# Optimization experiments

Measured on AMD Instinct MI355X. Metric: run time of the kernel, lower is better.

The kernel has to match this reference:

```python
import jax, jax.numpy as jnp
import numpy as np

N_NODES = 100000
N_EDGES = 1600000
D_IN = 128
D_HID = 128
D_OUT = 1
N_GRAPHS = 512


def setup_inputs() -> dict:
    key = jax.random.key(0)
    ks = jax.random.split(key, 12)
    x = jax.random.normal(ks[0], (N_NODES, D_IN), dtype=jnp.float32)
    edge_index = jax.random.randint(ks[1], (2, N_EDGES), 0, N_NODES, dtype=jnp.int32)
    batch = jnp.sort(jax.random.randint(ks[2], (N_NODES,), 0, N_GRAPHS, dtype=jnp.int32))

    def glorot(k, fan_in, fan_out):
        lim = jnp.sqrt(6.0 / (fan_in + fan_out)).astype(jnp.float32)
        return jax.random.uniform(k, (fan_in, fan_out), jnp.float32, -lim, lim)

    W1 = glorot(ks[3], D_IN, D_HID); b1 = jnp.zeros((D_HID,), jnp.float32)
    W2 = glorot(ks[4], D_HID, D_HID); b2 = jnp.zeros((D_HID,), jnp.float32)
    W3 = glorot(ks[5], D_HID, D_HID); b3 = jnp.zeros((D_HID,), jnp.float32)
    Wfc = glorot(ks[6], D_HID, D_OUT); bfc = jnp.zeros((D_OUT,), jnp.float32)
    return {"x": x, "edge_index": edge_index, "batch": batch,
            "W1": W1, "b1": b1, "W2": W2, "b2": b2, "W3": W3, "b3": b3,
            "Wfc": Wfc, "bfc": bfc}


def reference(x, edge_index, batch, W1, b1, W2, b2, W3, b3, Wfc, bfc):
    N = x.shape[0]
    src, dst = edge_index[0], edge_index[1]
    # GCN symmetric normalization with self-loops: deg = in-degree(A) + 1
    deg = jax.ops.segment_sum(jnp.ones_like(dst, dtype=x.dtype), dst, num_segments=N) + 1.0
    dis = jax.lax.rsqrt(deg)                       # deg^{-1/2}, [N]
    enorm = (dis[src] * dis[dst])[:, None]         # per-edge norm, [E,1]
    snorm = (dis * dis)[:, None]                   # self-loop norm, [N,1]

    def gcn_conv(h, W, b):
        h = h @ W                                  # transform first (standard GCNConv)
        agg = jax.ops.segment_sum(h[src] * enorm, dst, num_segments=N)
        return agg + h * snorm + b

    h = jax.nn.relu(gcn_conv(x, W1, b1))           # dropout p=0 (eval): identity
    h = jax.nn.relu(gcn_conv(h, W2, b2))
    h = jax.nn.relu(gcn_conv(h, W3, b3))

    # global_mean_pool over batch segments
    sums = jax.ops.segment_sum(h, batch, num_segments=N_GRAPHS)
    counts = jax.ops.segment_sum(jnp.ones((N, 1), h.dtype), batch, num_segments=N_GRAPHS)
    pooled = sums / jnp.maximum(counts, 1.0)       # [G, D_HID]
    return pooled @ Wfc + bfc                      # [G, 1]
```

## Files before the change

kernel.cpp:

```cpp
#include <hip/hip_runtime.h>

#define D 128
#define CHUNK 4096
#define SPAD 36

typedef unsigned int uint;
typedef __attribute__((ext_vector_type(8))) short short8;
typedef __attribute__((ext_vector_type(4))) float floatx4;

__device__ __forceinline__ float bf_lo(uint u) { return __uint_as_float(u << 16); }
__device__ __forceinline__ float bf_hi(uint u) { return __uint_as_float(u & 0xffff0000u); }
__device__ __forceinline__ uint f2bf(float f) {
    uint x = __float_as_uint(f);
    return (x + 0x7fffu + ((x >> 16) & 1u)) >> 16;
}


__global__ void init_cursor_kernel(int* __restrict__ cursor, int NB, int CAP) {
    int b = threadIdx.x + blockIdx.x * 128;
    if (b < NB) cursor[b] = b * CAP;
}

__global__ void bin_kernel(const int* __restrict__ src, const int* __restrict__ dst,
                           int* __restrict__ cursor, uint* __restrict__ binned, int E) {
    __shared__ int cnt[128];
    __shared__ int wcur[128];
    int t = threadIdx.x;
    if (t < 128) cnt[t] = 0;
    __syncthreads();
    int s0 = blockIdx.x * CHUNK;
    int e0 = min(s0 + CHUNK, E);
    for (int e = s0 + t; e < e0; e += 256)
        atomicAdd(&cnt[dst[e] >> 10], 1);
    __syncthreads();
    if (t < 128) {
        int c = cnt[t];
        wcur[t] = c ? atomicAdd(&cursor[t], c) : 0;
    }
    __syncthreads();
    for (int e = s0 + t; e < e0; e += 256) {
        int d = dst[e];
        int b = d >> 10;
        int p = atomicAdd(&wcur[b], 1);
        binned[p] = (uint)src[e] | ((uint)(d & 1023) << 17);
    }
}

__launch_bounds__(256)
__global__ void bucket_build_kernel(const uint* __restrict__ binned, const int* __restrict__ cursor,
                                    int* __restrict__ offs, int* __restrict__ oend,
                                    int* __restrict__ csr, float* __restrict__ dis,
                                    int N, int CAP) {
    __shared__ int hist[1024];
    __shared__ int tsum[256];
    __shared__ int wcur[1024];
    int b = blockIdx.x;
    int t = threadIdx.x;
    int s = b * CAP;
    int e = cursor[b];
    for (int i = t; i < 1024; i += 256) hist[i] = 0;
    __syncthreads();
    for (int i = s + t; i < e; i += 256)
        atomicAdd(&hist[(binned[i] >> 17) & 1023], 1);
    __syncthreads();
    int h0 = t * 4;
    int v0 = hist[h0], v1 = hist[h0 + 1], v2 = hist[h0 + 2], v3 = hist[h0 + 3];
    int ts = v0 + v1 + v2 + v3;
    tsum[t] = ts;
    __syncthreads();
    for (int off = 1; off < 256; off <<= 1) {
        int x = (t >= off) ? tsum[t - off] : 0;
        __syncthreads();
        tsum[t] += x;
        __syncthreads();
    }
    int excl = tsum[t] - ts;
    int o0 = excl, o1 = o0 + v0, o2 = o1 + v1, o3 = o2 + v2;
    int n0 = (b << 10) + h0;
    wcur[h0] = s + o0; wcur[h0 + 1] = s + o1; wcur[h0 + 2] = s + o2; wcur[h0 + 3] = s + o3;
    if (n0 < N)     { offs[n0]     = s + o0; oend[n0]     = s + o0 + v0; dis[n0]     = rsqrtf((float)v0 + 1.0f); }
    if (n0 + 1 < N) { offs[n0 + 1] = s + o1; oend[n0 + 1] = s + o1 + v1; dis[n0 + 1] = rsqrtf((float)v1 + 1.0f); }
    if (n0 + 2 < N) { offs[n0 + 2] = s + o2; oend[n0 + 2] = s + o2 + v2; dis[n0 + 2] = rsqrtf((float)v2 + 1.0f); }
    if (n0 + 3 < N) { offs[n0 + 3] = s + o3; oend[n0 + 3] = s + o3 + v3; dis[n0 + 3] = rsqrtf((float)v3 + 1.0f); }
    __syncthreads();
    for (int i = s + t; i < e; i += 256) {
        uint en = binned[i];
        int local = (en >> 17) & 1023;
        int p = atomicAdd(&wcur[local], 1);
        csr[p] = (int)(en & 0x1ffffu);
    }
}

__global__ void convert_wt_kernel(const float* __restrict__ W1, const float* __restrict__ W2,
                                  const float* __restrict__ W3, uint* __restrict__ Wt1,
                                  uint* __restrict__ Wt2, uint* __restrict__ Wt3) {
    int gidx = blockIdx.x * 256 + threadIdx.x;
    int w = gidx >> 13, rem = gidx & 8191;
    int n = rem >> 6, kp = rem & 63;
    const float* W = (w == 0) ? W1 : (w == 1) ? W2 : W3;
    uint* Wt = (w == 0) ? Wt1 : (w == 1) ? Wt2 : Wt3;
    Wt[(n << 6) + kp] = f2bf(W[(2 * kp) * 128 + n]) | (f2bf(W[(2 * kp + 1) * 128 + n]) << 16);
}

template <bool F32A>
__launch_bounds__(256)
__global__ void gemm_mfma_kernel(const void* __restrict__ Aptr, const uint* __restrict__ Wt,
                                 const float* __restrict__ dis, uint* __restrict__ U, int N) {
    __shared__ uint lds[128 * SPAD * 2];
    uint* a_lds = lds;
    uint* w_lds = lds + 128 * SPAD;
    int tid = threadIdx.x;
    int m0 = blockIdx.x * 128;
    int wave = tid >> 6, lane = tid & 63;
    int lm = lane & 15, quad = lane >> 4;

    floatx4 acc[2][8];
#pragma unroll
    for (int i = 0; i < 2; i++)
#pragma unroll
        for (int j = 0; j < 8; j++)
            acc[i][j] = (floatx4){0.f, 0.f, 0.f, 0.f};

    for (int ks = 0; ks < 2; ks++) {
        if (F32A) {
            const float* Af = (const float*)Aptr;
#pragma unroll
            for (int i = 0; i < 8; i++) {
                int gi = tid + i * 256;
                int row = gi >> 4, j = gi & 15;
                int grow = m0 + row;
                float4 v = (grow < N) ? *(const float4*)&Af[(size_t)grow * 128 + ks * 64 + j * 4]
                                      : make_float4(0.f, 0.f, 0.f, 0.f);
                uint2 o;
                o.x = f2bf(v.x) | (f2bf(v.y) << 16);
                o.y = f2bf(v.z) | (f2bf(v.w) << 16);
                *(uint2*)&a_lds[row * SPAD + j * 2] = o;
            }
        } else {
            const uint* Ab = (const uint*)Aptr;
#pragma unroll
            for (int i = 0; i < 4; i++) {
                int gi = tid + i * 256;
                int row = gi >> 3, c4 = (gi & 7) << 2;
                int grow = m0 + row;
                uint4 av = (grow < N) ? *(const uint4*)&Ab[(size_t)grow * 64 + ks * 32 + c4]
                                      : make_uint4(0u, 0u, 0u, 0u);
                *(uint4*)&a_lds[row * SPAD + c4] = av;
            }
        }
#pragma unroll
        for (int i = 0; i < 4; i++) {
            int gi = tid + i * 256;
            int row = gi >> 3, c4 = (gi & 7) << 2;
            *(uint4*)&w_lds[row * SPAD + c4] = *(const uint4*)&Wt[(size_t)row * 64 + ks * 32 + c4];
        }
        __syncthreads();
#pragma unroll
        for (int kc = 0; kc < 2; kc++) {
            int ko = kc * 16 + quad * 4;
            short8 b[8];
#pragma unroll
            for (int nt = 0; nt < 8; nt++)
                b[nt] = *(short8*)&w_lds[(nt * 16 + lm) * SPAD + ko];
            short8 a0 = *(short8*)&a_lds[(wave * 32 + lm) * SPAD + ko];
            short8 a1 = *(short8*)&a_lds[(wave * 32 + 16 + lm) * SPAD + ko];
#pragma unroll
            for (int nt = 0; nt < 8; nt++) {
                acc[0][nt] = __builtin_amdgcn_mfma_f32_16x16x32_bf16(a0, b[nt], acc[0][nt], 0, 0, 0);
                acc[1][nt] = __builtin_amdgcn_mfma_f32_16x16x32_bf16(a1, b[nt], acc[1][nt], 0, 0, 0);
            }
        }
        __syncthreads();
    }

    unsigned short* o_lds = (unsigned short*)lds;
    float dv[2][4];
#pragma unroll
    for (int ms = 0; ms < 2; ms++)
#pragma unroll
        for (int r = 0; r < 4; r++) {
            int row = m0 + wave * 32 + ms * 16 + quad * 4 + r;
            dv[ms][r] = (row < N) ? dis[row] : 0.f;
        }
#pragma unroll
    for (int ms = 0; ms < 2; ms++)
#pragma unroll
        for (int nt = 0; nt < 8; nt++)
#pragma unroll
            for (int r = 0; r < 4; r++) {
                int row = wave * 32 + ms * 16 + quad * 4 + r;
                int col = nt * 16 + lm;
                o_lds[row * 132 + col] = (unsigned short)f2bf(acc[ms][nt][r] * dv[ms][r]);
            }
    __syncthreads();
#pragma unroll
    for (int i = 0; i < 16; i++) {
        int gi = tid + i * 256;
        int row = gi >> 5, c2 = gi & 31;
        int grow = m0 + row;
        if (grow < N) {
            uint2 v = *(uint2*)&lds[row * 66 + c2 * 2];
            *(uint2*)&U[(size_t)grow * 64 + c2 * 2] = v;
        }
    }
}

__launch_bounds__(256)
__global__ void aggregate_kernel(const uint* __restrict__ U, const int* __restrict__ offs,
                                 const int* __restrict__ oend, const int* __restrict__ csr_src,
                                 const float* __restrict__ dis, const float* __restrict__ bias,
                                 uint* __restrict__ H, int N) {
    int wave = threadIdx.x >> 6;
    int lane = threadIdx.x & 63;
    int n = blockIdx.x * 4 + wave;
    if (n >= N) return;

    uint self = U[(size_t)n * 64 + lane];
    float accx = bf_lo(self);
    float accy = bf_hi(self);

    int s = offs[n], e = oend[n];
    int i = s;
    for (; i + 7 < e; i += 8) {
        int s0 = csr_src[i],     s1 = csr_src[i + 1], s2 = csr_src[i + 2], s3 = csr_src[i + 3];
        int s4 = csr_src[i + 4], s5 = csr_src[i + 5], s6 = csr_src[i + 6], s7 = csr_src[i + 7];
        uint u0 = U[(size_t)s0 * 64 + lane];
        uint u1 = U[(size_t)s1 * 64 + lane];
        uint u2 = U[(size_t)s2 * 64 + lane];
        uint u3 = U[(size_t)s3 * 64 + lane];
        uint u4 = U[(size_t)s4 * 64 + lane];
        uint u5 = U[(size_t)s5 * 64 + lane];
        uint u6 = U[(size_t)s6 * 64 + lane];
        uint u7 = U[(size_t)s7 * 64 + lane];
        accx += bf_lo(u0) + bf_lo(u1) + bf_lo(u2) + bf_lo(u3)
              + bf_lo(u4) + bf_lo(u5) + bf_lo(u6) + bf_lo(u7);
        accy += bf_hi(u0) + bf_hi(u1) + bf_hi(u2) + bf_hi(u3)
              + bf_hi(u4) + bf_hi(u5) + bf_hi(u6) + bf_hi(u7);
    }
    for (; i + 3 < e; i += 4) {
        int s0 = csr_src[i], s1 = csr_src[i + 1], s2 = csr_src[i + 2], s3 = csr_src[i + 3];
        uint u0 = U[(size_t)s0 * 64 + lane];
        uint u1 = U[(size_t)s1 * 64 + lane];
        uint u2 = U[(size_t)s2 * 64 + lane];
        uint u3 = U[(size_t)s3 * 64 + lane];
        accx += bf_lo(u0) + bf_lo(u1) + bf_lo(u2) + bf_lo(u3);
        accy += bf_hi(u0) + bf_hi(u1) + bf_hi(u2) + bf_hi(u3);
    }
    for (; i < e; i++) {
        uint u = U[(size_t)csr_src[i] * 64 + lane];
        accx += bf_lo(u);
        accy += bf_hi(u);
    }

    float dn = dis[n];
    float2 b = *(const float2*)&bias[lane * 2];
    float ox = fmaxf(fmaf(accx, dn, b.x), 0.0f);
    float oy = fmaxf(fmaf(accy, dn, b.y), 0.0f);
    H[(size_t)n * 64 + lane] = f2bf(ox) | (f2bf(oy) << 16);
}

__launch_bounds__(512)
__global__ void pool_fc_kernel(const uint* __restrict__ H, const int* __restrict__ batch,
                               const float* __restrict__ Wfc, const float* __restrict__ bfc,
                               float* __restrict__ out, int N) {
    __shared__ float2 red[512];
    int g = blockIdx.x;
    int t = threadIdx.x;
    int rid = t >> 6, lane = t & 63;

    int lo = 0, hi = N;
    while (lo < hi) { int mid = (lo + hi) >> 1; if (batch[mid] < g) lo = mid + 1; else hi = mid; }
    int st = lo;
    hi = N;
    while (lo < hi) { int mid = (lo + hi) >> 1; if (batch[mid] < g + 1) lo = mid + 1; else hi = mid; }
    int en = lo;

    float ax = 0.f, ay = 0.f;
    for (int r = st + rid; r < en; r += 8) {
        uint u = H[(size_t)r * 64 + lane];
        ax += bf_lo(u);
        ay += bf_hi(u);
    }
    red[t] = make_float2(ax, ay);
    __syncthreads();
    if (rid == 0) {
        float2 sv = red[lane];
#pragma unroll
        for (int i = 1; i < 8; i++) { sv.x += red[i * 64 + lane].x; sv.y += red[i * 64 + lane].y; }
        float cnt = fmaxf((float)(en - st), 1.0f);
        float p = (sv.x / cnt) * Wfc[lane * 2] + (sv.y / cnt) * Wfc[lane * 2 + 1];
        for (int off = 32; off > 0; off >>= 1) p += __shfl_down(p, off);
        if (lane == 0) out[g] = p + bfc[0];
    }
}

extern "C" void kernel_launch(void* const* d_in, const int* in_sizes, int n_in,
                              void* d_out, int out_size, void* d_ws, size_t ws_size,
                              hipStream_t stream) {
    const float* x   = (const float*)d_in[0];
    const int* eidx  = (const int*)d_in[1];
    const int* batch = (const int*)d_in[2];
    const float* W1  = (const float*)d_in[3];
    const float* b1  = (const float*)d_in[4];
    const float* W2  = (const float*)d_in[5];
    const float* b2  = (const float*)d_in[6];
    const float* W3  = (const float*)d_in[7];
    const float* b3  = (const float*)d_in[8];
    const float* Wfc = (const float*)d_in[9];
    const float* bfc = (const float*)d_in[10];
    float* out = (float*)d_out;

    int N = in_sizes[2];
    int E = in_sizes[1] / 2;
    int G = out_size;
    int NB = (N + 1023) >> 10;
    int CAP = E / NB + 2048;

    const int* src = eidx;
    const int* dst = eidx + E;

    char* ws = (char*)d_ws;
    size_t off = 0;
    auto alloc = [&](size_t bytes) -> void* {
        void* p = ws + off;
        off += (bytes + 255) & ~(size_t)255;
        return p;
    };
    size_t winsz = (size_t)NB * CAP;
    uint* U      = (uint*)alloc((size_t)N * 64 * sizeof(uint));
    uint* Hb     = (uint*)alloc((size_t)N * 64 * sizeof(uint));
    uint* Wt1    = (uint*)alloc(8192 * sizeof(uint));
    uint* Wt2    = (uint*)alloc(8192 * sizeof(uint));
    uint* Wt3    = (uint*)alloc(8192 * sizeof(uint));
    float* dis   = (float*)alloc((size_t)N * sizeof(float));
    int* offs    = (int*)alloc((size_t)N * sizeof(int));
    int* oend    = (int*)alloc((size_t)N * sizeof(int));
    int* csr     = (int*)alloc(winsz * sizeof(int));
    uint* binned = (uint*)alloc(winsz * sizeof(uint));
    int* cursor  = (int*)alloc(256 * sizeof(int));
    (void)ws_size; (void)n_in;

    int cb = (E + CHUNK - 1) / CHUNK;

    init_cursor_kernel<<<1, 128, 0, stream>>>(cursor, NB, CAP);
    bin_kernel<<<cb, 256, 0, stream>>>(src, dst, cursor, binned, E);
    bucket_build_kernel<<<NB, 256, 0, stream>>>(binned, cursor, offs, oend, csr, dis, N, CAP);

    convert_wt_kernel<<<96, 256, 0, stream>>>(W1, W2, W3, Wt1, Wt2, Wt3);

    int gb = (N + 127) / 128;
    int ab = (N + 3) / 4;

    gemm_mfma_kernel<true><<<gb, 256, 0, stream>>>(x, Wt1, dis, U, N);
    aggregate_kernel<<<ab, 256, 0, stream>>>(U, offs, oend, csr, dis, b1, Hb, N);
    gemm_mfma_kernel<false><<<gb, 256, 0, stream>>>(Hb, Wt2, dis, U, N);
    aggregate_kernel<<<ab, 256, 0, stream>>>(U, offs, oend, csr, dis, b2, Hb, N);
    gemm_mfma_kernel<false><<<gb, 256, 0, stream>>>(Hb, Wt3, dis, U, N);
    aggregate_kernel<<<ab, 256, 0, stream>>>(U, offs, oend, csr, dis, b3, Hb, N);
    pool_fc_kernel<<<G, 512, 0, stream>>>(Hb, batch, Wfc, bfc, out, N);
}
```

Baseline: 438.6 us.

## Fuse aggregation with next layer's GEMM and halve CSR bucket size

Layers 1 and 2 now do neighbour aggregation, bias and ReLU straight into shared memory, then run the next layer's MFMA GEMM in the same kernel. This removes the round trip of the hidden activations through global memory and two kernel launches. In exchange, each 128-row block gathers its rows serially (32 nodes per wave), and the fused kernel uses more shared memory, which may lower occupancy. The CSR binning also moves from 1024-node to 512-node buckets, giving more build blocks and smaller histograms.

```diff
diff --git a/kernel.cpp b/kernel.cpp
--- a/kernel.cpp
+++ b/kernel.cpp
@@ -3,8 +3,10 @@
 #define D 128
 #define CHUNK 4096
 #define SPAD 36
+#define SPADF 68
 
 typedef unsigned int uint;
+typedef unsigned short ushort;
 typedef __attribute__((ext_vector_type(8))) short short8;
 typedef __attribute__((ext_vector_type(4))) float floatx4;
 
@@ -17,32 +19,32 @@
 
 
 __global__ void init_cursor_kernel(int* __restrict__ cursor, int NB, int CAP) {
-    int b = threadIdx.x + blockIdx.x * 128;
+    int b = threadIdx.x;
     if (b < NB) cursor[b] = b * CAP;
 }
 
 __global__ void bin_kernel(const int* __restrict__ src, const int* __restrict__ dst,
                            int* __restrict__ cursor, uint* __restrict__ binned, int E) {
-    __shared__ int cnt[128];
-    __shared__ int wcur[128];
+    __shared__ int cnt[256];
+    __shared__ int wcur[256];
     int t = threadIdx.x;
-    if (t < 128) cnt[t] = 0;
+    cnt[t] = 0;
     __syncthreads();
     int s0 = blockIdx.x * CHUNK;
     int e0 = min(s0 + CHUNK, E);
     for (int e = s0 + t; e < e0; e += 256)
-        atomicAdd(&cnt[dst[e] >> 10], 1);
-    __syncthreads();
-    if (t < 128) {
+        atomicAdd(&cnt[dst[e] >> 9], 1);
+    __syncthreads();
+    {
         int c = cnt[t];
         wcur[t] = c ? atomicAdd(&cursor[t], c) : 0;
     }
     __syncthreads();
     for (int e = s0 + t; e < e0; e += 256) {
         int d = dst[e];
-        int b = d >> 10;
+        int b = d >> 9;
         int p = atomicAdd(&wcur[b], 1);
-        binned[p] = (uint)src[e] | ((uint)(d & 1023) << 17);
+        binned[p] = (uint)src[e] | ((uint)(d & 511) << 17);
     }
 }
 
@@ -51,21 +53,21 @@
                                     int* __restrict__ offs, int* __restrict__ oend,
                                     int* __restrict__ csr, float* __restrict__ dis,
                                     int N, int CAP) {
-    __shared__ int hist[1024];
+    __shared__ int hist[512];
     __shared__ int tsum[256];
-    __shared__ int wcur[1024];
+    __shared__ int wcur[512];
     int b = blockIdx.x;
     int t = threadIdx.x;
     int s = b * CAP;
     int e = cursor[b];
-    for (int i = t; i < 1024; i += 256) hist[i] = 0;
+    hist[t] = 0; hist[t + 256] = 0;
     __syncthreads();
     for (int i = s + t; i < e; i += 256)
-        atomicAdd(&hist[(binned[i] >> 17) & 1023], 1);
-    __syncthreads();
-    int h0 = t * 4;
-    int v0 = hist[h0], v1 = hist[h0 + 1], v2 = hist[h0 + 2], v3 = hist[h0 + 3];
-    int ts = v0 + v1 + v2 + v3;
+        atomicAdd(&hist[(binned[i] >> 17) & 511], 1);
+    __syncthreads();
+    int h0 = t * 2;
+    int v0 = hist[h0], v1 = hist[h0 + 1];
+    int ts = v0 + v1;
     tsum[t] = ts;
     __syncthreads();
     for (int off = 1; off < 256; off <<= 1) {
@@ -75,17 +77,15 @@
         __syncthreads();
     }
     int excl = tsum[t] - ts;
-    int o0 = excl, o1 = o0 + v0, o2 = o1 + v1, o3 = o2 + v2;
-    int n0 = (b << 10) + h0;
-    wcur[h0] = s + o0; wcur[h0 + 1] = s + o1; wcur[h0 + 2] = s + o2; wcur[h0 + 3] = s + o3;
+    int o0 = excl, o1 = o0 + v0;
+    int n0 = (b << 9) + h0;
+    wcur[h0] = s + o0; wcur[h0 + 1] = s + o1;
     if (n0 < N)     { offs[n0]     = s + o0; oend[n0]     = s + o0 + v0; dis[n0]     = rsqrtf((float)v0 + 1.0f); }
     if (n0 + 1 < N) { offs[n0 + 1] = s + o1; oend[n0 + 1] = s + o1 + v1; dis[n0 + 1] = rsqrtf((float)v1 + 1.0f); }
-    if (n0 + 2 < N) { offs[n0 + 2] = s + o2; oend[n0 + 2] = s + o2 + v2; dis[n0 + 2] = rsqrtf((float)v2 + 1.0f); }
-    if (n0 + 3 < N) { offs[n0 + 3] = s + o3; oend[n0 + 3] = s + o3 + v3; dis[n0 + 3] = rsqrtf((float)v3 + 1.0f); }
     __syncthreads();
     for (int i = s + t; i < e; i += 256) {
         uint en = binned[i];
-        int local = (en >> 17) & 1023;
+        int local = (en >> 17) & 511;
         int p = atomicAdd(&wcur[local], 1);
         csr[p] = (int)(en & 0x1ffffu);
     }
@@ -102,10 +102,9 @@
     Wt[(n << 6) + kp] = f2bf(W[(2 * kp) * 128 + n]) | (f2bf(W[(2 * kp + 1) * 128 + n]) << 16);
 }
 
-template <bool F32A>
 __launch_bounds__(256)
-__global__ void gemm_mfma_kernel(const void* __restrict__ Aptr, const uint* __restrict__ Wt,
-                                 const float* __restrict__ dis, uint* __restrict__ U, int N) {
+__global__ void gemm_mfma_f32_kernel(const float* __restrict__ Af, const uint* __restrict__ Wt,
+                                     const float* __restrict__ dis, uint* __restrict__ U, int N) {
     __shared__ uint lds[128 * SPAD * 2];
     uint* a_lds = lds;
     uint* w_lds = lds + 128 * SPAD;
@@ -122,31 +121,17 @@
             acc[i][j] = (floatx4){0.f, 0.f, 0.f, 0.f};
 
     for (int ks = 0; ks < 2; ks++) {
-        if (F32A) {
-            const float* Af = (const float*)Aptr;
-#pragma unroll
-            for (int i = 0; i < 8; i++) {
-                int gi = tid + i * 256;
-                int row = gi >> 4, j = gi & 15;
-                int grow = m0 + row;
-                float4 v = (grow < N) ? *(const float4*)&Af[(size_t)grow * 128 + ks * 64 + j * 4]
-                                      : make_float4(0.f, 0.f, 0.f, 0.f);
-                uint2 o;
-                o.x = f2bf(v.x) | (f2bf(v.y) << 16);
-                o.y = f2bf(v.z) | (f2bf(v.w) << 16);
-                *(uint2*)&a_lds[row * SPAD + j * 2] = o;
-            }
-        } else {
-            const uint* Ab = (const uint*)Aptr;
-#pragma unroll
-            for (int i = 0; i < 4; i++) {
-                int gi = tid + i * 256;
-                int row = gi >> 3, c4 = (gi & 7) << 2;
-                int grow = m0 + row;
-                uint4 av = (grow < N) ? *(const uint4*)&Ab[(size_t)grow * 64 + ks * 32 + c4]
-                                      : make_uint4(0u, 0u, 0u, 0u);
-                *(uint4*)&a_lds[row * SPAD + c4] = av;
-            }
+#pragma unroll
+        for (int i = 0; i < 8; i++) {
+            int gi = tid + i * 256;
+            int row = gi >> 4, j = gi & 15;
+            int grow = m0 + row;
+            float4 v = (grow < N) ? *(const float4*)&Af[(size_t)grow * 128 + ks * 64 + j * 4]
+                                  : make_float4(0.f, 0.f, 0.f, 0.f);
+            uint2 o;
+            o.x = f2bf(v.x) | (f2bf(v.y) << 16);
+            o.y = f2bf(v.z) | (f2bf(v.w) << 16);
+            *(uint2*)&a_lds[row * SPAD + j * 2] = o;
         }
 #pragma unroll
         for (int i = 0; i < 4; i++) {
@@ -173,7 +158,7 @@
         __syncthreads();
     }
 
-    unsigned short* o_lds = (unsigned short*)lds;
+    ushort* o_lds = (ushort*)lds;
     float dv[2][4];
 #pragma unroll
     for (int ms = 0; ms < 2; ms++)
@@ -190,7 +175,7 @@
             for (int r = 0; r < 4; r++) {
                 int row = wave * 32 + ms * 16 + quad * 4 + r;
                 int col = nt * 16 + lm;
-                o_lds[row * 132 + col] = (unsigned short)f2bf(acc[ms][nt][r] * dv[ms][r]);
+                o_lds[row * 132 + col] = (ushort)f2bf(acc[ms][nt][r] * dv[ms][r]);
             }
     __syncthreads();
 #pragma unroll
@@ -201,6 +186,130 @@
         if (grow < N) {
             uint2 v = *(uint2*)&lds[row * 66 + c2 * 2];
             *(uint2*)&U[(size_t)grow * 64 + c2 * 2] = v;
+        }
+    }
+}
+
+__launch_bounds__(256)
+__global__ void agg_gemm_kernel(const uint* __restrict__ U, const int* __restrict__ offs,
+                                const int* __restrict__ oend, const int* __restrict__ csr_src,
+                                const float* __restrict__ dis, const float* __restrict__ bias,
+                                const uint* __restrict__ Wt, uint* __restrict__ Unext, int N) {
+    __shared__ uint lds[128 * SPADF * 2];
+    uint* a_lds = lds;
+    uint* w_lds = lds + 128 * SPADF;
+    int tid = threadIdx.x;
+    int m0 = blockIdx.x * 128;
+    int wave = tid >> 6, lane = tid & 63;
+
+#pragma unroll
+    for (int i = 0; i < 8; i++) {
+        int gi = tid + i * 256;
+        int row = gi >> 4, c4 = (gi & 15) << 2;
+        *(uint4*)&w_lds[row * SPADF + c4] = *(const uint4*)&Wt[(size_t)row * 64 + c4];
+    }
+
+    float2 bv = *(const float2*)&bias[lane * 2];
+    for (int i = 0; i < 32; i++) {
+        int r = wave * 32 + i;
+        int n = m0 + r;
+        uint pk = 0;
+        if (n < N) {
+            uint self = U[(size_t)n * 64 + lane];
+            float accx = bf_lo(self), accy = bf_hi(self);
+            int s = offs[n], e = oend[n];
+            int j = s;
+            for (; j + 7 < e; j += 8) {
+                int s0 = csr_src[j],     s1 = csr_src[j + 1], s2 = csr_src[j + 2], s3 = csr_src[j + 3];
+                int s4 = csr_src[j + 4], s5 = csr_src[j + 5], s6 = csr_src[j + 6], s7 = csr_src[j + 7];
+                uint u0 = U[(size_t)s0 * 64 + lane];
+                uint u1 = U[(size_t)s1 * 64 + lane];
+                uint u2 = U[(size_t)s2 * 64 + lane];
+                uint u3 = U[(size_t)s3 * 64 + lane];
+                uint u4 = U[(size_t)s4 * 64 + lane];
+                uint u5 = U[(size_t)s5 * 64 + lane];
+                uint u6 = U[(size_t)s6 * 64 + lane];
+                uint u7 = U[(size_t)s7 * 64 + lane];
+                accx += bf_lo(u0) + bf_lo(u1) + bf_lo(u2) + bf_lo(u3)
+                      + bf_lo(u4) + bf_lo(u5) + bf_lo(u6) + bf_lo(u7);
+                accy += bf_hi(u0) + bf_hi(u1) + bf_hi(u2) + bf_hi(u3)
+                      + bf_hi(u4) + bf_hi(u5) + bf_hi(u6) + bf_hi(u7);
+            }
+            for (; j + 3 < e; j += 4) {
+                int s0 = csr_src[j], s1 = csr_src[j + 1], s2 = csr_src[j + 2], s3 = csr_src[j + 3];
+                uint u0 = U[(size_t)s0 * 64 + lane];
+                uint u1 = U[(size_t)s1 * 64 + lane];
+                uint u2 = U[(size_t)s2 * 64 + lane];
+                uint u3 = U[(size_t)s3 * 64 + lane];
+                accx += bf_lo(u0) + bf_lo(u1) + bf_lo(u2) + bf_lo(u3);
+                accy += bf_hi(u0) + bf_hi(u1) + bf_hi(u2) + bf_hi(u3);
+            }
+            for (; j < e; j++) {
+                uint u = U[(size_t)csr_src[j] * 64 + lane];
+                accx += bf_lo(u);
+                accy += bf_hi(u);
+            }
+            float dn = dis[n];
+            float ox = fmaxf(fmaf(accx, dn, bv.x), 0.0f);
+            float oy = fmaxf(fmaf(accy, dn, bv.y), 0.0f);
+            pk = f2bf(ox) | (f2bf(oy) << 16);
+        }
+        a_lds[r * SPADF + lane] = pk;
+    }
+    __syncthreads();
+
+    int lm = lane & 15, quad = lane >> 4;
+    floatx4 acc[2][8];
+#pragma unroll
+    for (int i = 0; i < 2; i++)
+#pragma unroll
+        for (int j = 0; j < 8; j++)
+            acc[i][j] = (floatx4){0.f, 0.f, 0.f, 0.f};
+#pragma unroll
+    for (int kc = 0; kc < 4; kc++) {
+        int ko = kc * 16 + quad * 4;
+        short8 b[8];
+#pragma unroll
+        for (int nt = 0; nt < 8; nt++)
+            b[nt] = *(short8*)&w_lds[(nt * 16 + lm) * SPADF + ko];
+        short8 a0 = *(short8*)&a_lds[(wave * 32 + lm) * SPADF + ko];
+        short8 a1 = *(short8*)&a_lds[(wave * 32 + 16 + lm) * SPADF + ko];
+#pragma unroll
+        for (int nt = 0; nt < 8; nt++) {
+            acc[0][nt] = __builtin_amdgcn_mfma_f32_16x16x32_bf16(a0, b[nt], acc[0][nt], 0, 0, 0);
+            acc[1][nt] = __builtin_amdgcn_mfma_f32_16x16x32_bf16(a1, b[nt], acc[1][nt], 0, 0, 0);
+        }
+    }
+    __syncthreads();
+
+    ushort* o_lds = (ushort*)lds;
+    float dv[2][4];
+#pragma unroll
+    for (int ms = 0; ms < 2; ms++)
+#pragma unroll
+        for (int r = 0; r < 4; r++) {
+            int row = m0 + wave * 32 + ms * 16 + quad * 4 + r;
+            dv[ms][r] = (row < N) ? dis[row] : 0.f;
+        }
+#pragma unroll
+    for (int ms = 0; ms < 2; ms++)
+#pragma unroll
+        for (int nt = 0; nt < 8; nt++)
+#pragma unroll
+            for (int r = 0; r < 4; r++) {
+                int row = wave * 32 + ms * 16 + quad * 4 + r;
+                int col = nt * 16 + lm;
+                o_lds[row * 132 + col] = (ushort)f2bf(acc[ms][nt][r] * dv[ms][r]);
+            }
+    __syncthreads();
+#pragma unroll
+    for (int i = 0; i < 16; i++) {
+        int gi = tid + i * 256;
+        int row = gi >> 5, c2 = gi & 31;
+        int grow = m0 + row;
+        if (grow < N) {
+            uint2 v = *(uint2*)&lds[row * 66 + c2 * 2];
+            *(uint2*)&Unext[(size_t)grow * 64 + c2 * 2] = v;
         }
     }
 }
@@ -313,8 +422,8 @@
     int N = in_sizes[2];
     int E = in_sizes[1] / 2;
     int G = out_size;
-    int NB = (N + 1023) >> 10;
-    int CAP = E / NB + 2048;
+    int NB = (N + 511) >> 9;
+    int CAP = E / NB + 1536;
 
     const int* src = eidx;
     const int* dst = eidx + E;
@@ -327,8 +436,8 @@
         return p;
     };
     size_t winsz = (size_t)NB * CAP;
-    uint* U      = (uint*)alloc((size_t)N * 64 * sizeof(uint));
-    uint* Hb     = (uint*)alloc((size_t)N * 64 * sizeof(uint));
+    uint* Ua     = (uint*)alloc((size_t)N * 64 * sizeof(uint));
+    uint* Ub     = (uint*)alloc((size_t)N * 64 * sizeof(uint));
     uint* Wt1    = (uint*)alloc(8192 * sizeof(uint));
     uint* Wt2    = (uint*)alloc(8192 * sizeof(uint));
     uint* Wt3    = (uint*)alloc(8192 * sizeof(uint));
@@ -342,7 +451,7 @@
 
     int cb = (E + CHUNK - 1) / CHUNK;
 
-    init_cursor_kernel<<<1, 128, 0, stream>>>(cursor, NB, CAP);
+    init_cursor_kernel<<<1, 256, 0, stream>>>(cursor, NB, CAP);
     bin_kernel<<<cb, 256, 0, stream>>>(src, dst, cursor, binned, E);
     bucket_build_kernel<<<NB, 256, 0, stream>>>(binned, cursor, offs, oend, csr, dis, N, CAP);
 
@@ -351,11 +460,9 @@
     int gb = (N + 127) / 128;
     int ab = (N + 3) / 4;
 
-    gemm_mfma_kernel<true><<<gb, 256, 0, stream>>>(x, Wt1, dis, U, N);
-    aggregate_kernel<<<ab, 256, 0, stream>>>(U, offs, oend, csr, dis, b1, Hb, N);
-    gemm_mfma_kernel<false><<<gb, 256, 0, stream>>>(Hb, Wt2, dis, U, N);
-    aggregate_kernel<<<ab, 256, 0, stream>>>(U, offs, oend, csr, dis, b2, Hb, N);
-    gemm_mfma_kernel<false><<<gb, 256, 0, stream>>>(Hb, Wt3, dis, U, N);
-    aggregate_kernel<<<ab, 256, 0, stream>>>(U, offs, oend, csr, dis, b3, Hb, N);
-    pool_fc_kernel<<<G, 512, 0, stream>>>(Hb, batch, Wfc, bfc, out, N);
-}
+    gemm_mfma_f32_kernel<<<gb, 256, 0, stream>>>(x, Wt1, dis, Ua, N);
+    agg_gemm_kernel<<<gb, 256, 0, stream>>>(Ua, offs, oend, csr, dis, b1, Wt2, Ub, N);
+    agg_gemm_kernel<<<gb, 256, 0, stream>>>(Ub, offs, oend, csr, dis, b2, Wt3, Ua, N);
+    aggregate_kernel<<<ab, 256, 0, stream>>>(Ua, offs, oend, csr, dis, b3, Ub, N);
+    pool_fc_kernel<<<G, 512, 0, stream>>>(Ub, batch, Wfc, bfc, out, N);
+}
```

After: 651.0 us. 1.48x slower.

## Vectorize neighbor gather with 16-lane groups and shrink CSR buckets

Applied to the files above, without the earlier changes.

The aggregation kernel now splits each wave into four 16-lane groups. Each group loads a different neighbor row with 128-bit loads, and the partial sums are combined with cross-lane shuffles before the self-loop, bias and ReLU are applied. This is meant to raise memory-level parallelism and cut per-edge instruction overhead in the latency-bound random gather. The CSR build also switches from 1024-node to 512-node buckets, giving the bucket build stage more blocks and smaller shared-memory histograms. The cost is extra shuffle work and uneven group loads for low-degree nodes.

```diff
diff --git a/kernel.cpp b/kernel.cpp
--- a/kernel.cpp
+++ b/kernel.cpp
@@ -5,6 +5,7 @@
 #define SPAD 36
 
 typedef unsigned int uint;
+typedef unsigned short ushort;
 typedef __attribute__((ext_vector_type(8))) short short8;
 typedef __attribute__((ext_vector_type(4))) float floatx4;
 
@@ -17,32 +18,32 @@
 
 
 __global__ void init_cursor_kernel(int* __restrict__ cursor, int NB, int CAP) {
-    int b = threadIdx.x + blockIdx.x * 128;
+    int b = threadIdx.x;
     if (b < NB) cursor[b] = b * CAP;
 }
 
 __global__ void bin_kernel(const int* __restrict__ src, const int* __restrict__ dst,
                            int* __restrict__ cursor, uint* __restrict__ binned, int E) {
-    __shared__ int cnt[128];
-    __shared__ int wcur[128];
+    __shared__ int cnt[256];
+    __shared__ int wcur[256];
     int t = threadIdx.x;
-    if (t < 128) cnt[t] = 0;
+    cnt[t] = 0;
     __syncthreads();
     int s0 = blockIdx.x * CHUNK;
     int e0 = min(s0 + CHUNK, E);
     for (int e = s0 + t; e < e0; e += 256)
-        atomicAdd(&cnt[dst[e] >> 10], 1);
-    __syncthreads();
-    if (t < 128) {
+        atomicAdd(&cnt[dst[e] >> 9], 1);
+    __syncthreads();
+    {
         int c = cnt[t];
         wcur[t] = c ? atomicAdd(&cursor[t], c) : 0;
     }
     __syncthreads();
     for (int e = s0 + t; e < e0; e += 256) {
         int d = dst[e];
-        int b = d >> 10;
+        int b = d >> 9;
         int p = atomicAdd(&wcur[b], 1);
-        binned[p] = (uint)src[e] | ((uint)(d & 1023) << 17);
+        binned[p] = (uint)src[e] | ((uint)(d & 511) << 17);
     }
 }
 
@@ -51,21 +52,21 @@
                                     int* __restrict__ offs, int* __restrict__ oend,
                                     int* __restrict__ csr, float* __restrict__ dis,
                                     int N, int CAP) {
-    __shared__ int hist[1024];
+    __shared__ int hist[512];
     __shared__ int tsum[256];
-    __shared__ int wcur[1024];
+    __shared__ int wcur[512];
     int b = blockIdx.x;
     int t = threadIdx.x;
     int s = b * CAP;
     int e = cursor[b];
-    for (int i = t; i < 1024; i += 256) hist[i] = 0;
+    hist[t] = 0; hist[t + 256] = 0;
     __syncthreads();
     for (int i = s + t; i < e; i += 256)
-        atomicAdd(&hist[(binned[i] >> 17) & 1023], 1);
-    __syncthreads();
-    int h0 = t * 4;
-    int v0 = hist[h0], v1 = hist[h0 + 1], v2 = hist[h0 + 2], v3 = hist[h0 + 3];
-    int ts = v0 + v1 + v2 + v3;
+        atomicAdd(&hist[(binned[i] >> 17) & 511], 1);
+    __syncthreads();
+    int h0 = t * 2;
+    int v0 = hist[h0], v1 = hist[h0 + 1];
+    int ts = v0 + v1;
     tsum[t] = ts;
     __syncthreads();
     for (int off = 1; off < 256; off <<= 1) {
@@ -75,17 +76,15 @@
         __syncthreads();
     }
     int excl = tsum[t] - ts;
-    int o0 = excl, o1 = o0 + v0, o2 = o1 + v1, o3 = o2 + v2;
-    int n0 = (b << 10) + h0;
-    wcur[h0] = s + o0; wcur[h0 + 1] = s + o1; wcur[h0 + 2] = s + o2; wcur[h0 + 3] = s + o3;
+    int o0 = excl, o1 = o0 + v0;
+    int n0 = (b << 9) + h0;
+    wcur[h0] = s + o0; wcur[h0 + 1] = s + o1;
     if (n0 < N)     { offs[n0]     = s + o0; oend[n0]     = s + o0 + v0; dis[n0]     = rsqrtf((float)v0 + 1.0f); }
     if (n0 + 1 < N) { offs[n0 + 1] = s + o1; oend[n0 + 1] = s + o1 + v1; dis[n0 + 1] = rsqrtf((float)v1 + 1.0f); }
-    if (n0 + 2 < N) { offs[n0 + 2] = s + o2; oend[n0 + 2] = s + o2 + v2; dis[n0 + 2] = rsqrtf((float)v2 + 1.0f); }
-    if (n0 + 3 < N) { offs[n0 + 3] = s + o3; oend[n0 + 3] = s + o3 + v3; dis[n0 + 3] = rsqrtf((float)v3 + 1.0f); }
     __syncthreads();
     for (int i = s + t; i < e; i += 256) {
         uint en = binned[i];
-        int local = (en >> 17) & 1023;
+        int local = (en >> 17) & 511;
         int p = atomicAdd(&wcur[local], 1);
         csr[p] = (int)(en & 0x1ffffu);
     }
@@ -173,7 +172,7 @@
         __syncthreads();
     }
 
-    unsigned short* o_lds = (unsigned short*)lds;
+    ushort* o_lds = (ushort*)lds;
     float dv[2][4];
 #pragma unroll
     for (int ms = 0; ms < 2; ms++)
@@ -190,7 +189,7 @@
             for (int r = 0; r < 4; r++) {
                 int row = wave * 32 + ms * 16 + quad * 4 + r;
                 int col = nt * 16 + lm;
-                o_lds[row * 132 + col] = (unsigned short)f2bf(acc[ms][nt][r] * dv[ms][r]);
+                o_lds[row * 132 + col] = (ushort)f2bf(acc[ms][nt][r] * dv[ms][r]);
             }
     __syncthreads();
 #pragma unroll
@@ -214,49 +213,59 @@
     int lane = threadIdx.x & 63;
     int n = blockIdx.x * 4 + wave;
     if (n >= N) return;
-
-    uint self = U[(size_t)n * 64 + lane];
-    float accx = bf_lo(self);
-    float accy = bf_hi(self);
-
+    int g = lane >> 4, i16 = lane & 15;
+
+    float a0 = 0.f, a1 = 0.f, a2 = 0.f, a3 = 0.f, a4 = 0.f, a5 = 0.f, a6 = 0.f, a7 = 0.f;
     int s = offs[n], e = oend[n];
-    int i = s;
-    for (; i + 7 < e; i += 8) {
-        int s0 = csr_src[i],     s1 = csr_src[i + 1], s2 = csr_src[i + 2], s3 = csr_src[i + 3];
-        int s4 = csr_src[i + 4], s5 = csr_src[i + 5], s6 = csr_src[i + 6], s7 = csr_src[i + 7];
-        uint u0 = U[(size_t)s0 * 64 + lane];
-        uint u1 = U[(size_t)s1 * 64 + lane];
-        uint u2 = U[(size_t)s2 * 64 + lane];
-        uint u3 = U[(size_t)s3 * 64 + lane];
-        uint u4 = U[(size_t)s4 * 64 + lane];
-        uint u5 = U[(size_t)s5 * 64 + lane];
-        uint u6 = U[(size_t)s6 * 64 + lane];
-        uint u7 = U[(size_t)s7 * 64 + lane];
-        accx += bf_lo(u0) + bf_lo(u1) + bf_lo(u2) + bf_lo(u3)
-              + bf_lo(u4) + bf_lo(u5) + bf_lo(u6) + bf_lo(u7);
-        accy += bf_hi(u0) + bf_hi(u1) + bf_hi(u2) + bf_hi(u3)
-              + bf_hi(u4) + bf_hi(u5) + bf_hi(u6) + bf_hi(u7);
-    }
-    for (; i + 3 < e; i += 4) {
-        int s0 = csr_src[i], s1 = csr_src[i + 1], s2 = csr_src[i + 2], s3 = csr_src[i + 3];
-        uint u0 = U[(size_t)s0 * 64 + lane];
-        uint u1 = U[(size_t)s1 * 64 + lane];
-        uint u2 = U[(size_t)s2 * 64 + lane];
-        uint u3 = U[(size_t)s3 * 64 + lane];
-        accx += bf_lo(u0) + bf_lo(u1) + bf_lo(u2) + bf_lo(u3);
-        accy += bf_hi(u0) + bf_hi(u1) + bf_hi(u2) + bf_hi(u3);
-    }
-    for (; i < e; i++) {
-        uint u = U[(size_t)csr_src[i] * 64 + lane];
-        accx += bf_lo(u);
-        accy += bf_hi(u);
-    }
-
-    float dn = dis[n];
-    float2 b = *(const float2*)&bias[lane * 2];
-    float ox = fmaxf(fmaf(accx, dn, b.x), 0.0f);
-    float oy = fmaxf(fmaf(accy, dn, b.y), 0.0f);
-    H[(size_t)n * 64 + lane] = f2bf(ox) | (f2bf(oy) << 16);
+    int j = s + g;
+    for (; j + 12 < e; j += 16) {
+        int s0 = csr_src[j], s1 = csr_src[j + 4], s2 = csr_src[j + 8], s3 = csr_src[j + 12];
+        uint4 u0 = *(const uint4*)&U[(size_t)s0 * 64 + i16 * 4];
+        uint4 u1 = *(const uint4*)&U[(size_t)s1 * 64 + i16 * 4];
+        uint4 u2 = *(const uint4*)&U[(size_t)s2 * 64 + i16 * 4];
+        uint4 u3 = *(const uint4*)&U[(size_t)s3 * 64 + i16 * 4];
+        a0 += bf_lo(u0.x) + bf_lo(u1.x) + bf_lo(u2.x) + bf_lo(u3.x);
+        a1 += bf_hi(u0.x) + bf_hi(u1.x) + bf_hi(u2.x) + bf_hi(u3.x);
+        a2 += bf_lo(u0.y) + bf_lo(u1.y) + bf_lo(u2.y) + bf_lo(u3.y);
+        a3 += bf_hi(u0.y) + bf_hi(u1.y) + bf_hi(u2.y) + bf_hi(u3.y);
+        a4 += bf_lo(u0.z) + bf_lo(u1.z) + bf_lo(u2.z) + bf_lo(u3.z);
+        a5 += bf_hi(u0.z) + bf_hi(u1.z) + bf_hi(u2.z) + bf_hi(u3.z);
+        a6 += bf_lo(u0.w) + bf_lo(u1.w) + bf_lo(u2.w) + bf_lo(u3.w);
+        a7 += bf_hi(u0.w) + bf_hi(u1.w) + bf_hi(u2.w) + bf_hi(u3.w);
+    }
+    for (; j < e; j += 4) {
+        int s0 = csr_src[j];
+        uint4 u = *(const uint4*)&U[(size_t)s0 * 64 + i16 * 4];
+        a0 += bf_lo(u.x); a1 += bf_hi(u.x);
+        a2 += bf_lo(u.y); a3 += bf_hi(u.y);
+        a4 += bf_lo(u.z); a5 += bf_hi(u.z);
+        a6 += bf_lo(u.w); a7 += bf_hi(u.w);
+    }
+    a0 += __shfl_xor(a0, 16); a0 += __shfl_xor(a0, 32);
+    a1 += __shfl_xor(a1, 16); a1 += __shfl_xor(a1, 32);
+    a2 += __shfl_xor(a2, 16); a2 += __shfl_xor(a2, 32);
+    a3 += __shfl_xor(a3, 16); a3 += __shfl_xor(a3, 32);
+    a4 += __shfl_xor(a4, 16); a4 += __shfl_xor(a4, 32);
+    a5 += __shfl_xor(a5, 16); a5 += __shfl_xor(a5, 32);
+    a6 += __shfl_xor(a6, 16); a6 += __shfl_xor(a6, 32);
+    a7 += __shfl_xor(a7, 16); a7 += __shfl_xor(a7, 32);
+
+    if (g == 0) {
+        uint4 su = *(const uint4*)&U[(size_t)n * 64 + i16 * 4];
+        a0 += bf_lo(su.x); a1 += bf_hi(su.x);
+        a2 += bf_lo(su.y); a3 += bf_hi(su.y);
+        a4 += bf_lo(su.z); a5 += bf_hi(su.z);
+        a6 += bf_lo(su.w); a7 += bf_hi(su.w);
+        float dn = dis[n];
+        float4 b0 = *(const float4*)&bias[i16 * 8];
+        float4 b1 = *(const float4*)&bias[i16 * 8 + 4];
+        uint4 o;
+        o.x = f2bf(fmaxf(fmaf(a0, dn, b0.x), 0.f)) | (f2bf(fmaxf(fmaf(a1, dn, b0.y), 0.f)) << 16);
+        o.y = f2bf(fmaxf(fmaf(a2, dn, b0.z), 0.f)) | (f2bf(fmaxf(fmaf(a3, dn, b0.w), 0.f)) << 16);
+        o.z = f2bf(fmaxf(fmaf(a4, dn, b1.x), 0.f)) | (f2bf(fmaxf(fmaf(a5, dn, b1.y), 0.f)) << 16);
+        o.w = f2bf(fmaxf(fmaf(a6, dn, b1.z), 0.f)) | (f2bf(fmaxf(fmaf(a7, dn, b1.w), 0.f)) << 16);
+        *(uint4*)&H[(size_t)n * 64 + i16 * 4] = o;
+    }
 }
 
 __launch_bounds__(512)
@@ -313,8 +322,8 @@
     int N = in_sizes[2];
     int E = in_sizes[1] / 2;
     int G = out_size;
-    int NB = (N + 1023) >> 10;
-    int CAP = E / NB + 2048;
+    int NB = (N + 511) >> 9;
+    int CAP = E / NB + 1536;
 
     const int* src = eidx;
     const int* dst = eidx + E;
@@ -327,8 +336,8 @@
         return p;
     };
     size_t winsz = (size_t)NB * CAP;
-    uint* U      = (uint*)alloc((size_t)N * 64 * sizeof(uint));
-    uint* Hb     = (uint*)alloc((size_t)N * 64 * sizeof(uint));
+    uint* Ua     = (uint*)alloc((size_t)N * 64 * sizeof(uint));
+    uint* Ub     = (uint*)alloc((size_t)N * 64 * sizeof(uint));
     uint* Wt1    = (uint*)alloc(8192 * sizeof(uint));
     uint* Wt2    = (uint*)alloc(8192 * sizeof(uint));
     uint* Wt3    = (uint*)alloc(8192 * sizeof(uint));
@@ -342,7 +351,7 @@
 
     int cb = (E + CHUNK - 1) / CHUNK;
 
-    init_cursor_kernel<<<1, 128, 0, stream>>>(cursor, NB, CAP);
+    init_cursor_kernel<<<1, 256, 0, stream>>>(cursor, NB, CAP);
     bin_kernel<<<cb, 256, 0, stream>>>(src, dst, cursor, binned, E);
     bucket_build_kernel<<<NB, 256, 0, stream>>>(binned, cursor, offs, oend, csr, dis, N, CAP);
 
@@ -351,11 +360,11 @@
     int gb = (N + 127) / 128;
     int ab = (N + 3) / 4;
 
-    gemm_mfma_kernel<true><<<gb, 256, 0, stream>>>(x, Wt1, dis, U, N);
-    aggregate_kernel<<<ab, 256, 0, stream>>>(U, offs, oend, csr, dis, b1, Hb, N);
-    gemm_mfma_kernel<false><<<gb, 256, 0, stream>>>(Hb, Wt2, dis, U, N);
-    aggregate_kernel<<<ab, 256, 0, stream>>>(U, offs, oend, csr, dis, b2, Hb, N);
-    gemm_mfma_kernel<false><<<gb, 256, 0, stream>>>(Hb, Wt3, dis, U, N);
-    aggregate_kernel<<<ab, 256, 0, stream>>>(U, offs, oend, csr, dis, b3, Hb, N);
-    pool_fc_kernel<<<G, 512, 0, stream>>>(Hb, batch, Wfc, bfc, out, N);
-}
+    gemm_mfma_kernel<true><<<gb, 256, 0, stream>>>(x, Wt1, dis, Ua, N);
+    aggregate_kernel<<<ab, 256, 0, stream>>>(Ua, offs, oend, csr, dis, b1, Ub, N);
+    gemm_mfma_kernel<false><<<gb, 256, 0, stream>>>(Ub, Wt2, dis, Ua, N);
+    aggregate_kernel<<<ab, 256, 0, stream>>>(Ua, offs, oend, csr, dis, b2, Ub, N);
+    gemm_mfma_kernel<false><<<gb, 256, 0, stream>>>(Ub, Wt3, dis, Ua, N);
+    aggregate_kernel<<<ab, 256, 0, stream>>>(Ua, offs, oend, csr, dis, b3, Ub, N);
+    pool_fc_kernel<<<G, 512, 0, stream>>>(Ub, batch, Wfc, bfc, out, N);
+}
```

Result: faster. 420.7 us (-4.1%).
